# Optimization experiments

Measured on AMD Instinct MI355X. Metric: run time of the kernel, lower is better.

## Reference

```python
import jax, jax.numpy as jnp
import numpy as np

N_NODES = 50000
N_EDGES = 800000
IN_CH = 128
HEADS = 4
HID = 32  # per-head dim; heads*hid = 128
N_GRAPHS = 128


def setup_inputs() -> dict:
    key = jax.random.key(0)
    ks = jax.random.split(key, 32)
    d = {}
    d["x"] = jax.random.normal(ks[0], (N_NODES, IN_CH), dtype=jnp.float32)
    d["edge_index"] = jax.random.randint(ks[1], (2, N_EDGES), 0, N_NODES, dtype=jnp.int64)
    d["batch"] = jnp.sort(jax.random.randint(ks[2], (N_NODES,), 0, N_GRAPHS, dtype=jnp.int64))
    HD = HEADS * HID
    names = [("wq1", (IN_CH, HD)), ("bq1", (HD,)), ("wk1", (IN_CH, HD)), ("bk1", (HD,)),
             ("wv1", (IN_CH, HD)), ("bv1", (HD,)), ("ws1", (IN_CH, HD)), ("bs1", (HD,)),
             ("wq2", (HD, HD)), ("bq2", (HD,)), ("wk2", (HD, HD)), ("bk2", (HD,)),
             ("wv2", (HD, HD)), ("bv2", (HD,)), ("ws2", (HD, HD)), ("bs2", (HD,)),
             ("wl", (HD, HD)), ("bl", (HD,)), ("wl2", (HD, 1)), ("bl2", (1,))]
    for i, (nm, shp) in enumerate(names):
        d[nm] = jax.random.normal(ks[3 + i], shp, dtype=jnp.float32) * 0.05
    return d


def _transformer_conv(x, src, dst, wq, bq, wk, bk, wv, bv, ws, bs):
    """PyG TransformerConv: multi-head dot-product attention over edges,
    softmax normalized per destination node, plus linear root/skip term."""
    N = x.shape[0]
    q = (x @ wq + bq).reshape(N, HEADS, HID)
    k = (x @ wk + bk).reshape(N, HEADS, HID)
    v = (x @ wv + bv).reshape(N, HEADS, HID)
    # edge scores: [E, H]
    e = jnp.einsum('ehd,ehd->eh', q[dst], k[src]) * np.float32(1.0 / np.sqrt(HID))
    # segment softmax over incoming edges of each destination node
    m = jax.ops.segment_max(e, dst, num_segments=N)
    a = jnp.exp(e - m[dst])
    s = jax.ops.segment_sum(a, dst, num_segments=N)
    alpha = a / s[dst]  # [E, H]
    msg = alpha[:, :, None] * v[src]  # [E, H, D]
    out = jax.ops.segment_sum(msg, dst, num_segments=N).reshape(N, HEADS * HID)
    return out + x @ ws + bs  # root weight (skip) term


def reference(x, edge_index, batch,
              wq1, bq1, wk1, bk1, wv1, bv1, ws1, bs1,
              wq2, bq2, wk2, bk2, wv2, bv2, ws2, bs2,
              wl, bl, wl2, bl2):
    src, dst = edge_index[0], edge_index[1]
    h = _transformer_conv(x, src, dst, wq1, bq1, wk1, bk1, wv1, bv1, ws1, bs1)
    h = jax.nn.relu(h)
    h = _transformer_conv(h, src, dst, wq2, bq2, wk2, bk2, wv2, bv2, ws2, bs2)
    h = jax.nn.relu(h)
    h = h @ wl + bl
    h = h @ wl2 + bl2  # [N, 1]
    # global mean pool over graphs
    sums = jax.ops.segment_sum(h, batch, num_segments=N_GRAPHS)
    cnts = jax.ops.segment_sum(jnp.ones((h.shape[0], 1), h.dtype), batch, num_segments=N_GRAPHS)
    return sums / jnp.maximum(cnts, 1.0)
```

## Files before the change

kernel.cpp:

```cpp
#include <hip/hip_runtime.h>
#include <hip/hip_bf16.h>
#include <math.h>

#define NNODES 50000
#define NEDGES 800000
#define NGRAPHS 128
#define SCAN_B ((NNODES + 255) / 256)

typedef __attribute__((ext_vector_type(8))) short bf16x8;
typedef __attribute__((ext_vector_type(4))) float f32x4;

__device__ __forceinline__ unsigned short f2bf(float f) {
    unsigned int u = __float_as_uint(f);
    return (unsigned short)((u + 0x7FFFu + ((u >> 16) & 1u)) >> 16);
}
__device__ __forceinline__ unsigned pack2bf(float a, float b) {
    return (unsigned)f2bf(a) | ((unsigned)f2bf(b) << 16);
}
__device__ __forceinline__ float2 bf2f2(unsigned int u) {
    float2 f;
    f.x = __uint_as_float(u << 16);
    f.y = __uint_as_float(u & 0xFFFF0000u);
    return f;
}

__global__ void count_edges(const int* __restrict__ ei, int* __restrict__ cnt) {
    int e = blockIdx.x * 256 + threadIdx.x;
    if (e < NEDGES) atomicAdd(&cnt[ei[NEDGES + e]], 1);
}

__global__ __launch_bounds__(256)
void scan_pass1(const int* __restrict__ cnt, int* __restrict__ bsum) {
    const int t = threadIdx.x;
    const int i = blockIdx.x * 256 + t;
    int v = (i < NNODES) ? cnt[i] : 0;
#pragma unroll
    for (int off = 32; off > 0; off >>= 1) v += __shfl_xor(v, off, 64);
    __shared__ int ws[4];
    if ((t & 63) == 0) ws[t >> 6] = v;
    __syncthreads();
    if (t == 0) bsum[blockIdx.x] = ws[0] + ws[1] + ws[2] + ws[3];
}

__global__ __launch_bounds__(256)
void scan_pass2(const int* __restrict__ bsum, int* __restrict__ boff) {
    const int t = threadIdx.x;
    const int v = (t < SCAN_B) ? bsum[t] : 0;
    __shared__ int a[256];
    a[t] = v;
    __syncthreads();
    for (int off = 1; off < 256; off <<= 1) {
        const int u = (t >= off) ? a[t - off] : 0;
        __syncthreads();
        a[t] += u;
        __syncthreads();
    }
    if (t < SCAN_B) boff[t] = a[t] - v;
}

__global__ __launch_bounds__(256)
void scan_pass3(const int* __restrict__ cnt, const int* __restrict__ boff,
                int* __restrict__ rowptr, int* __restrict__ wpos) {
    const int t = threadIdx.x;
    const int i = blockIdx.x * 256 + t;
    const int v = (i < NNODES) ? cnt[i] : 0;
    __shared__ int a[256];
    a[t] = v;
    __syncthreads();
    for (int off = 1; off < 256; off <<= 1) {
        const int u = (t >= off) ? a[t - off] : 0;
        __syncthreads();
        a[t] += u;
        __syncthreads();
    }
    if (i < NNODES) {
        const int e = boff[blockIdx.x] + a[t] - v;
        rowptr[i] = e;
        wpos[i]   = e;
    }
    if (i == 0) rowptr[NNODES] = NEDGES;
}

__global__ void fill_csr(const int* __restrict__ ei, int* __restrict__ wpos,
                         int* __restrict__ colsrc) {
    int e = blockIdx.x * 256 + threadIdx.x;
    if (e < NEDGES) {
        int d = ei[NEDGES + e];
        int slot = atomicAdd(&wpos[d], 1);
        colsrc[slot] = ei[e];
    }
}

__global__ __launch_bounds__(256)
void prep_all(const float* __restrict__ wq1, const float* __restrict__ wk1,
              const float* __restrict__ wv1, const float* __restrict__ ws1,
              const float* __restrict__ wq2, const float* __restrict__ wk2,
              const float* __restrict__ wv2, const float* __restrict__ ws2,
              const float* __restrict__ wl, const float* __restrict__ bl,
              const float* __restrict__ wl2, const float* __restrict__ bl2,
              unsigned short* __restrict__ Wt, float* __restrict__ wf,
              float* __restrict__ bf) {
    const int b = blockIdx.x;
    if (b < 512) {
        const int layer = b >> 8;
        const int sel   = (b >> 6) & 3;
        const float* W = layer == 0
            ? (sel == 0 ? wq1 : sel == 1 ? wk1 : sel == 2 ? wv1 : ws1)
            : (sel == 0 ? wq2 : sel == 1 ? wk2 : sel == 2 ? wv2 : ws2);
        const int idx = (b & 63) * 256 + threadIdx.x;
        const int col = idx & 127;
        const int k   = idx >> 7;
        Wt[layer * 65536 + sel * 16384 + col * 128 + k] = f2bf(W[k * 128 + col]);
    } else {
        const int g = (b - 512) * 4 + (threadIdx.x >> 6);
        const int l = threadIdx.x & 63;
        if (g <= 128) {
            const float* row = (g < 128) ? &wl[g * 128] : bl;
            float s = row[l] * wl2[l] + row[64 + l] * wl2[64 + l];
#pragma unroll
            for (int off = 32; off > 0; off >>= 1) s += __shfl_xor(s, off, 64);
            if (l == 0) {
                if (g < 128) wf[g] = s;
                else         bf[0] = s + bl2[0];
            }
        }
    }
}

template <bool A_BF16>
__global__ __launch_bounds__(256, 3)
void gemm_qkvs(const void* __restrict__ Fv, const unsigned short* __restrict__ Wt,
               const float* __restrict__ bq, const float* __restrict__ bk,
               const float* __restrict__ bv, const float* __restrict__ bsk,
               unsigned short* __restrict__ Qb, unsigned short* __restrict__ Kb,
               unsigned short* __restrict__ Vb, unsigned short* __restrict__ Hb) {
    __shared__ __align__(16) unsigned short As[128][136];
    const int t    = threadIdx.x;
    const int m0   = blockIdx.x * 128;
    const int lane = t & 63;
    const int w    = t >> 6;
    const int l15  = lane & 15;
    const int lg   = lane >> 4;

    {
        const int row = t >> 1;
        const int kh  = (t & 1) * 64;
        const int gr  = min(m0 + row, NNODES - 1);
        if constexpr (A_BF16) {
            const unsigned short* src = &((const unsigned short*)Fv)[(size_t)gr * 128 + kh];
#pragma unroll
            for (int p = 0; p < 8; ++p)
                *(uint4*)&As[row][kh + p * 8] = *(const uint4*)&src[p * 8];
        } else {
            const float* src = &((const float*)Fv)[(size_t)gr * 128 + kh];
#pragma unroll
            for (int p = 0; p < 16; ++p) {
                const float4 v = *(const float4*)&src[p * 4];
                ushort4 u;
                u.x = f2bf(v.x); u.y = f2bf(v.y); u.z = f2bf(v.z); u.w = f2bf(v.w);
                *(ushort4*)&As[row][kh + p * 4] = u;
            }
        }
    }
    __syncthreads();

    for (int sl = 0; sl < 8; ++sl) {
        const int sel = sl >> 1;
        const int c0  = (sl & 1) * 64;
        const float* bias = sel == 0 ? bq : sel == 1 ? bk : sel == 2 ? bv : bsk;
        unsigned short* Ob = sel == 0 ? Qb : sel == 1 ? Kb : sel == 2 ? Vb : Hb;
        const unsigned short* Wsel = Wt + sel * 16384 + (size_t)c0 * 128;

        const float b0 = bias[c0 + l15];
        const float b1 = bias[c0 + 16 + l15];
        const float b2 = bias[c0 + 32 + l15];
        const float b3 = bias[c0 + 48 + l15];
        f32x4 a00 = {b0, b0, b0, b0}, a01 = {b1, b1, b1, b1},
              a02 = {b2, b2, b2, b2}, a03 = {b3, b3, b3, b3};
        f32x4 a10 = a00, a11 = a01, a12 = a02, a13 = a03;
#pragma unroll
        for (int ks = 0; ks < 4; ++ks) {
            const int kof = ks * 32 + lg * 8;
            const bf16x8 af0 = *(const bf16x8*)&As[w * 32 + l15][kof];
            const bf16x8 af1 = *(const bf16x8*)&As[w * 32 + 16 + l15][kof];
            const bf16x8 bf0 = *(const bf16x8*)&Wsel[(size_t)(l15) * 128 + kof];
            const bf16x8 bf1 = *(const bf16x8*)&Wsel[(size_t)(16 + l15) * 128 + kof];
            const bf16x8 bf2 = *(const bf16x8*)&Wsel[(size_t)(32 + l15) * 128 + kof];
            const bf16x8 bf3 = *(const bf16x8*)&Wsel[(size_t)(48 + l15) * 128 + kof];
            a00 = __builtin_amdgcn_mfma_f32_16x16x32_bf16(af0, bf0, a00, 0, 0, 0);
            a01 = __builtin_amdgcn_mfma_f32_16x16x32_bf16(af0, bf1, a01, 0, 0, 0);
            a02 = __builtin_amdgcn_mfma_f32_16x16x32_bf16(af0, bf2, a02, 0, 0, 0);
            a03 = __builtin_amdgcn_mfma_f32_16x16x32_bf16(af0, bf3, a03, 0, 0, 0);
            a10 = __builtin_amdgcn_mfma_f32_16x16x32_bf16(af1, bf0, a10, 0, 0, 0);
            a11 = __builtin_amdgcn_mfma_f32_16x16x32_bf16(af1, bf1, a11, 0, 0, 0);
            a12 = __builtin_amdgcn_mfma_f32_16x16x32_bf16(af1, bf2, a12, 0, 0, 0);
            a13 = __builtin_amdgcn_mfma_f32_16x16x32_bf16(af1, bf3, a13, 0, 0, 0);
        }

        const int r0 = m0 + w * 32 + lg * 4;
#define STB(ACC, RT, CT)                                                       \
        _Pragma("unroll")                                                      \
        for (int i = 0; i < 4; ++i) {                                          \
            const int gr = r0 + (RT) * 16 + i;                                 \
            if (gr < NNODES)                                                   \
                Ob[(size_t)gr * 128 + c0 + (CT) * 16 + l15] = f2bf(ACC[i]);    \
        }
        STB(a00, 0, 0) STB(a01, 0, 1) STB(a02, 0, 2) STB(a03, 0, 3)
        STB(a10, 1, 0) STB(a11, 1, 1) STB(a12, 1, 2) STB(a13, 1, 3)
#undef STB
    }
}

template <bool FUSE_HEAD>
__global__ __launch_bounds__(128)
void attn_agg(const unsigned short* __restrict__ Qb,
              const unsigned short* __restrict__ Kb,
              const unsigned short* __restrict__ Vb,
              unsigned short* __restrict__ Hb,
              const int* __restrict__ rowptr, const int* __restrict__ colsrc,
              const float* __restrict__ wf, float* __restrict__ r) {
    const int n = blockIdx.x * 2 + (threadIdx.x >> 6);
    const int l = threadIdx.x & 63;
    const int e = l >> 4;
    const int c = (l & 15) * 8;
    const uint4 qu = *(const uint4*)&Qb[(size_t)n * 128 + c];
    const float S = 0.17677669529663687f * 1.4426950408889634f;
    const float2 t01 = bf2f2(qu.x), t23 = bf2f2(qu.y);
    const float2 t45 = bf2f2(qu.z), t67 = bf2f2(qu.w);
    const float q0 = t01.x * S, q1 = t01.y * S, q2 = t23.x * S, q3 = t23.y * S;
    const float q4 = t45.x * S, q5 = t45.y * S, q6 = t67.x * S, q7 = t67.y * S;
    const int beg = rowptr[n], end = rowptr[n + 1];
    const int cnt = end - beg;

    float m = -INFINITY, s = 0.f;
    float a0 = 0.f, a1 = 0.f, a2 = 0.f, a3 = 0.f;
    float a4 = 0.f, a5 = 0.f, a6 = 0.f, a7 = 0.f;

    uint4 ku, vu;
    if (cnt > 0) {
        const int src = colsrc[min(beg + e, end - 1)];
        ku = *(const uint4*)&Kb[(size_t)src * 128 + c];
        vu = *(const uint4*)&Vb[(size_t)src * 128 + c];
    }
    for (int i = beg; i < end; i += 4) {
        const uint4 kc = ku, vc = vu;
        const bool valid = (i + e) < end;
        if (i + 4 < end) {
            const int srcN = colsrc[min(i + 4 + e, end - 1)];
            ku = *(const uint4*)&Kb[(size_t)srcN * 128 + c];
            vu = *(const uint4*)&Vb[(size_t)srcN * 128 + c];
        }
        const float2 k01 = bf2f2(kc.x), k23 = bf2f2(kc.y);
        const float2 k45 = bf2f2(kc.z), k67 = bf2f2(kc.w);
        float p = q0 * k01.x;
        p = fmaf(q1, k01.y, p); p = fmaf(q2, k23.x, p); p = fmaf(q3, k23.y, p);
        p = fmaf(q4, k45.x, p); p = fmaf(q5, k45.y, p); p = fmaf(q6, k67.x, p);
        p = fmaf(q7, k67.y, p);
        p += __shfl_xor(p, 2);
        p += __shfl_xor(p, 1);
        if (!valid) p = -INFINITY;
        if (!__all(p <= m + 8.f)) {
            float pm = fmaxf(p, __shfl_xor(p, 16));
            pm = fmaxf(pm, __shfl_xor(pm, 32));
            const float nm = fmaxf(m, pm);
            const float sc = exp2f(m - nm);
            s *= sc;
            a0 *= sc; a1 *= sc; a2 *= sc; a3 *= sc;
            a4 *= sc; a5 *= sc; a6 *= sc; a7 *= sc;
            m = nm;
        }
        const float w = exp2f(p - m);
        s += w;
        const float2 v01 = bf2f2(vc.x), v23 = bf2f2(vc.y);
        const float2 v45 = bf2f2(vc.z), v67 = bf2f2(vc.w);
        a0 = fmaf(w, v01.x, a0); a1 = fmaf(w, v01.y, a1);
        a2 = fmaf(w, v23.x, a2); a3 = fmaf(w, v23.y, a3);
        a4 = fmaf(w, v45.x, a4); a5 = fmaf(w, v45.y, a5);
        a6 = fmaf(w, v67.x, a6); a7 = fmaf(w, v67.y, a7);
    }
    s  += __shfl_xor(s, 16);  s  += __shfl_xor(s, 32);
    a0 += __shfl_xor(a0, 16); a0 += __shfl_xor(a0, 32);
    a1 += __shfl_xor(a1, 16); a1 += __shfl_xor(a1, 32);
    a2 += __shfl_xor(a2, 16); a2 += __shfl_xor(a2, 32);
    a3 += __shfl_xor(a3, 16); a3 += __shfl_xor(a3, 32);
    a4 += __shfl_xor(a4, 16); a4 += __shfl_xor(a4, 32);
    a5 += __shfl_xor(a5, 16); a5 += __shfl_xor(a5, 32);
    a6 += __shfl_xor(a6, 16); a6 += __shfl_xor(a6, 32);
    a7 += __shfl_xor(a7, 16); a7 += __shfl_xor(a7, 32);

    const uint4 hu = *(const uint4*)&Hb[(size_t)n * 128 + c];
    const float2 h01 = bf2f2(hu.x), h23 = bf2f2(hu.y);
    const float2 h45 = bf2f2(hu.z), h67 = bf2f2(hu.w);
    float o0 = h01.x, o1 = h01.y, o2 = h23.x, o3 = h23.y;
    float o4 = h45.x, o5 = h45.y, o6 = h67.x, o7 = h67.y;
    if (cnt > 0) {
        const float inv = 1.f / s;
        o0 = fmaf(a0, inv, o0); o1 = fmaf(a1, inv, o1);
        o2 = fmaf(a2, inv, o2); o3 = fmaf(a3, inv, o3);
        o4 = fmaf(a4, inv, o4); o5 = fmaf(a5, inv, o5);
        o6 = fmaf(a6, inv, o6); o7 = fmaf(a7, inv, o7);
    }
    o0 = fmaxf(o0, 0.f); o1 = fmaxf(o1, 0.f); o2 = fmaxf(o2, 0.f);
    o3 = fmaxf(o3, 0.f); o4 = fmaxf(o4, 0.f); o5 = fmaxf(o5, 0.f);
    o6 = fmaxf(o6, 0.f); o7 = fmaxf(o7, 0.f);
    if (!FUSE_HEAD) {
        if (e == 0) {
            uint4 o;
            o.x = pack2bf(o0, o1); o.y = pack2bf(o2, o3);
            o.z = pack2bf(o4, o5); o.w = pack2bf(o6, o7);
            *(uint4*)&Hb[(size_t)n * 128 + c] = o;
        }
    } else {
        const float4 wA = *(const float4*)&wf[c];
        const float4 wB = *(const float4*)&wf[c + 4];
        float val = fmaf(o0, wA.x, fmaf(o1, wA.y, fmaf(o2, wA.z, o3 * wA.w)));
        val = fmaf(o4, wB.x, fmaf(o5, wB.y, fmaf(o6, wB.z, fmaf(o7, wB.w, val))));
        val += __shfl_xor(val, 8);
        val += __shfl_xor(val, 4);
        val += __shfl_xor(val, 2);
        val += __shfl_xor(val, 1);
        if (l == 0) r[n] = val;
    }
}

__global__ __launch_bounds__(256)
void graph_pool(const float* __restrict__ r, const int* __restrict__ batch,
                const float* __restrict__ bf, float* __restrict__ out) {
    const int g = blockIdx.x;
    const int t = threadIdx.x;
    int lo = 0, hi = NNODES;
    while (lo < hi) { int mid = (lo + hi) >> 1; if (batch[mid] < g) lo = mid + 1; else hi = mid; }
    const int beg = lo;
    lo = beg; hi = NNODES;
    while (lo < hi) { int mid = (lo + hi) >> 1; if (batch[mid] < g + 1) lo = mid + 1; else hi = mid; }
    const int end = lo;

    float s = 0.f;
    for (int i = beg + t; i < end; i += 256) s += r[i];
#pragma unroll
    for (int off = 32; off > 0; off >>= 1) s += __shfl_xor(s, off, 64);
    __shared__ float pw[4];
    if ((t & 63) == 0) pw[t >> 6] = s;
    __syncthreads();
    if (t == 0) {
        const float cnt = (float)(end - beg);
        const float tot = pw[0] + pw[1] + pw[2] + pw[3] + cnt * bf[0];
        out[g] = tot / fmaxf(cnt, 1.f);
    }
}

extern "C" void kernel_launch(void* const* d_in, const int* in_sizes, int n_in,
                              void* d_out, int out_size, void* d_ws, size_t ws_size,
                              hipStream_t stream) {
    const float* x     = (const float*)d_in[0];
    const int*   ei    = (const int*)d_in[1];
    const int*   batch = (const int*)d_in[2];
    const float* wq1 = (const float*)d_in[3];  const float* bq1 = (const float*)d_in[4];
    const float* wk1 = (const float*)d_in[5];  const float* bk1 = (const float*)d_in[6];
    const float* wv1 = (const float*)d_in[7];  const float* bv1 = (const float*)d_in[8];
    const float* ws1 = (const float*)d_in[9];  const float* bs1 = (const float*)d_in[10];
    const float* wq2 = (const float*)d_in[11]; const float* bq2 = (const float*)d_in[12];
    const float* wk2 = (const float*)d_in[13]; const float* bk2 = (const float*)d_in[14];
    const float* wv2 = (const float*)d_in[15]; const float* bv2 = (const float*)d_in[16];
    const float* ws2 = (const float*)d_in[17]; const float* bs2 = (const float*)d_in[18];
    const float* wl  = (const float*)d_in[19]; const float* bl  = (const float*)d_in[20];
    const float* wl2 = (const float*)d_in[21]; const float* bl2 = (const float*)d_in[22];

    char* wsb = (char*)d_ws;
    size_t off = 0;
    auto carve = [&](size_t bytes) -> void* {
        void* p = wsb + off;
        off = (off + bytes + 255) & ~(size_t)255;
        return p;
    };
    const size_t NB = (size_t)NNODES * 128 * 2;
    unsigned short* Qb = (unsigned short*)carve(NB);
    unsigned short* Kb = (unsigned short*)carve(NB);
    unsigned short* Vb = (unsigned short*)carve(NB);
    unsigned short* H1 = (unsigned short*)carve(NB);
    unsigned short* H2 = (unsigned short*)carve(NB);
    int*   rowptr = (int*)carve((NNODES + 1) * sizeof(int));
    int*   wpos   = (int*)carve(NNODES * sizeof(int));
    int*   cnt    = (int*)carve(NNODES * sizeof(int));
    int*   colsrc = (int*)carve(NEDGES * sizeof(int));
    int*   bsum   = (int*)carve(256 * sizeof(int));
    int*   boff   = (int*)carve(256 * sizeof(int));
    float* wf     = (float*)carve(129 * sizeof(float));
    float* bf     = wf + 128;
    float* nodeval = (float*)carve(NNODES * sizeof(float));
    unsigned short* Wt = (unsigned short*)carve(131072 * sizeof(unsigned short));

    hipMemsetAsync(cnt, 0, NNODES * sizeof(int), stream);

    count_edges<<<(NEDGES + 255) / 256, 256, 0, stream>>>(ei, cnt);
    scan_pass1<<<SCAN_B, 256, 0, stream>>>(cnt, bsum);
    scan_pass2<<<1, 256, 0, stream>>>(bsum, boff);
    scan_pass3<<<SCAN_B, 256, 0, stream>>>(cnt, boff, rowptr, wpos);
    fill_csr<<<(NEDGES + 255) / 256, 256, 0, stream>>>(ei, wpos, colsrc);
    prep_all<<<545, 256, 0, stream>>>(wq1, wk1, wv1, ws1, wq2, wk2, wv2, ws2,
                                      wl, bl, wl2, bl2, Wt, wf, bf);

    const int ggrid = (NNODES + 127) / 128;
    const int agrid = NNODES / 2;
    gemm_qkvs<false><<<ggrid, 256, 0, stream>>>(x, Wt, bq1, bk1, bv1, bs1,
                                                Qb, Kb, Vb, H1);
    attn_agg<false><<<agrid, 128, 0, stream>>>(Qb, Kb, Vb, H1, rowptr, colsrc,
                                               nullptr, nullptr);
    gemm_qkvs<true><<<ggrid, 256, 0, stream>>>(H1, Wt + 65536, bq2, bk2, bv2, bs2,
                                               Qb, Kb, Vb, H2);
    attn_agg<true><<<agrid, 128, 0, stream>>>(Qb, Kb, Vb, H2, rowptr, colsrc,
                                              wf, nodeval);
    graph_pool<<<NGRAPHS, 256, 0, stream>>>(nodeval, batch, bf, (float*)d_out);
}
```

Before: 397.9 us.

## Fuse CSR build into one cooperative kernel and stage GEMM weights in LDS

Replaces the memset plus five CSR-building launches (count, three-pass scan, fill) with a single cooperative kernel that uses grid-wide syncs between phases, cutting launch overhead and small-kernel gaps. Separately, the QKVS GEMM now double-buffers each 64-column weight slice into shared memory instead of reading B fragments directly from global memory, and drops the occupancy hint from launch bounds. The extra LDS (two 64x136 bf16 buffers) and a barrier per slice may lower occupancy. The cooperative grid of 196 blocks must be co-resident for the grid syncs to work.

```diff
diff --git a/kernel.cpp b/kernel.cpp
--- a/kernel.cpp
+++ b/kernel.cpp
@@ -1,6 +1,9 @@
 #include <hip/hip_runtime.h>
 #include <hip/hip_bf16.h>
+#include <hip/hip_cooperative_groups.h>
 #include <math.h>
+
+namespace cg = cooperative_groups;
 
 #define NNODES 50000
 #define NEDGES 800000
@@ -24,29 +27,24 @@
     return f;
 }
 
-__global__ void count_edges(const int* __restrict__ ei, int* __restrict__ cnt) {
-    int e = blockIdx.x * 256 + threadIdx.x;
-    if (e < NEDGES) atomicAdd(&cnt[ei[NEDGES + e]], 1);
-}
-
 __global__ __launch_bounds__(256)
-void scan_pass1(const int* __restrict__ cnt, int* __restrict__ bsum) {
+void build_csr(const int* __restrict__ ei, int* __restrict__ cnt,
+               int* __restrict__ bsum, int* __restrict__ rowptr,
+               int* __restrict__ wpos, int* __restrict__ colsrc) {
+    cg::grid_group grid = cg::this_grid();
     const int t = threadIdx.x;
-    const int i = blockIdx.x * 256 + t;
-    int v = (i < NNODES) ? cnt[i] : 0;
-#pragma unroll
-    for (int off = 32; off > 0; off >>= 1) v += __shfl_xor(v, off, 64);
-    __shared__ int ws[4];
-    if ((t & 63) == 0) ws[t >> 6] = v;
-    __syncthreads();
-    if (t == 0) bsum[blockIdx.x] = ws[0] + ws[1] + ws[2] + ws[3];
-}
-
-__global__ __launch_bounds__(256)
-void scan_pass2(const int* __restrict__ bsum, int* __restrict__ boff) {
-    const int t = threadIdx.x;
-    const int v = (t < SCAN_B) ? bsum[t] : 0;
+    const int gid = blockIdx.x * 256 + t;
+    const int gstride = gridDim.x * 256;
+
+    for (int i = gid; i < NNODES; i += gstride) cnt[i] = 0;
+    grid.sync();
+
+    for (int e = gid; e < NEDGES; e += gstride)
+        atomicAdd(&cnt[ei[NEDGES + e]], 1);
+    grid.sync();
+
     __shared__ int a[256];
+    const int v = (gid < NNODES) ? cnt[gid] : 0;
     a[t] = v;
     __syncthreads();
     for (int off = 1; off < 256; off <<= 1) {
@@ -55,38 +53,28 @@
         a[t] += u;
         __syncthreads();
     }
-    if (t < SCAN_B) boff[t] = a[t] - v;
-}
-
-__global__ __launch_bounds__(256)
-void scan_pass3(const int* __restrict__ cnt, const int* __restrict__ boff,
-                int* __restrict__ rowptr, int* __restrict__ wpos) {
-    const int t = threadIdx.x;
-    const int i = blockIdx.x * 256 + t;
-    const int v = (i < NNODES) ? cnt[i] : 0;
-    __shared__ int a[256];
-    a[t] = v;
+    if (t == 255) bsum[blockIdx.x] = a[255];
+    grid.sync();
+
+    int s = 0;
+    for (int j = t; j < blockIdx.x; j += 256) s += bsum[j];
+#pragma unroll
+    for (int off = 32; off > 0; off >>= 1) s += __shfl_xor(s, off, 64);
+    __shared__ int pw[4];
+    if ((t & 63) == 0) pw[t >> 6] = s;
     __syncthreads();
-    for (int off = 1; off < 256; off <<= 1) {
-        const int u = (t >= off) ? a[t - off] : 0;
-        __syncthreads();
-        a[t] += u;
-        __syncthreads();
-    }
-    if (i < NNODES) {
-        const int e = boff[blockIdx.x] + a[t] - v;
-        rowptr[i] = e;
-        wpos[i]   = e;
-    }
-    if (i == 0) rowptr[NNODES] = NEDGES;
-}
-
-__global__ void fill_csr(const int* __restrict__ ei, int* __restrict__ wpos,
-                         int* __restrict__ colsrc) {
-    int e = blockIdx.x * 256 + threadIdx.x;
-    if (e < NEDGES) {
-        int d = ei[NEDGES + e];
-        int slot = atomicAdd(&wpos[d], 1);
+    const int boff = pw[0] + pw[1] + pw[2] + pw[3];
+    if (gid < NNODES) {
+        const int e = boff + a[t] - v;
+        rowptr[gid] = e;
+        wpos[gid]   = e;
+    }
+    if (gid == 0) rowptr[NNODES] = NEDGES;
+    grid.sync();
+
+    for (int e = gid; e < NEDGES; e += gstride) {
+        const int d = ei[NEDGES + e];
+        const int slot = atomicAdd(&wpos[d], 1);
         colsrc[slot] = ei[e];
     }
 }
@@ -128,13 +116,14 @@
 }
 
 template <bool A_BF16>
-__global__ __launch_bounds__(256, 3)
+__global__ __launch_bounds__(256)
 void gemm_qkvs(const void* __restrict__ Fv, const unsigned short* __restrict__ Wt,
                const float* __restrict__ bq, const float* __restrict__ bk,
                const float* __restrict__ bv, const float* __restrict__ bsk,
                unsigned short* __restrict__ Qb, unsigned short* __restrict__ Kb,
                unsigned short* __restrict__ Vb, unsigned short* __restrict__ Hb) {
     __shared__ __align__(16) unsigned short As[128][136];
+    __shared__ __align__(16) unsigned short Bt[2][64][136];
     const int t    = threadIdx.x;
     const int m0   = blockIdx.x * 128;
     const int lane = t & 63;
@@ -162,14 +151,28 @@
             }
         }
     }
+
+#define STAGE_B(BUF, SL)                                                       \
+    {                                                                          \
+        const int sel_ = (SL) >> 1, c0_ = ((SL) & 1) * 64;                     \
+        const int col = t >> 2, kb = (t & 3) * 32;                             \
+        const unsigned short* src = &Wt[sel_ * 16384 + (c0_ + col) * 128 + kb];\
+        _Pragma("unroll")                                                      \
+        for (int p = 0; p < 4; ++p)                                            \
+            *(uint4*)&Bt[BUF][col][kb + p * 8] = *(const uint4*)&src[p * 8];   \
+    }
+
+    STAGE_B(0, 0)
     __syncthreads();
 
     for (int sl = 0; sl < 8; ++sl) {
+        const int cur = sl & 1;
+        if (sl < 7) STAGE_B(cur ^ 1, sl + 1)
+
         const int sel = sl >> 1;
         const int c0  = (sl & 1) * 64;
         const float* bias = sel == 0 ? bq : sel == 1 ? bk : sel == 2 ? bv : bsk;
         unsigned short* Ob = sel == 0 ? Qb : sel == 1 ? Kb : sel == 2 ? Vb : Hb;
-        const unsigned short* Wsel = Wt + sel * 16384 + (size_t)c0 * 128;
 
         const float b0 = bias[c0 + l15];
         const float b1 = bias[c0 + 16 + l15];
@@ -183,10 +186,10 @@
             const int kof = ks * 32 + lg * 8;
             const bf16x8 af0 = *(const bf16x8*)&As[w * 32 + l15][kof];
             const bf16x8 af1 = *(const bf16x8*)&As[w * 32 + 16 + l15][kof];
-            const bf16x8 bf0 = *(const bf16x8*)&Wsel[(size_t)(l15) * 128 + kof];
-            const bf16x8 bf1 = *(const bf16x8*)&Wsel[(size_t)(16 + l15) * 128 + kof];
-            const bf16x8 bf2 = *(const bf16x8*)&Wsel[(size_t)(32 + l15) * 128 + kof];
-            const bf16x8 bf3 = *(const bf16x8*)&Wsel[(size_t)(48 + l15) * 128 + kof];
+            const bf16x8 bf0 = *(const bf16x8*)&Bt[cur][l15][kof];
+            const bf16x8 bf1 = *(const bf16x8*)&Bt[cur][16 + l15][kof];
+            const bf16x8 bf2 = *(const bf16x8*)&Bt[cur][32 + l15][kof];
+            const bf16x8 bf3 = *(const bf16x8*)&Bt[cur][48 + l15][kof];
             a00 = __builtin_amdgcn_mfma_f32_16x16x32_bf16(af0, bf0, a00, 0, 0, 0);
             a01 = __builtin_amdgcn_mfma_f32_16x16x32_bf16(af0, bf1, a01, 0, 0, 0);
             a02 = __builtin_amdgcn_mfma_f32_16x16x32_bf16(af0, bf2, a02, 0, 0, 0);
@@ -208,7 +211,9 @@
         STB(a00, 0, 0) STB(a01, 0, 1) STB(a02, 0, 2) STB(a03, 0, 3)
         STB(a10, 1, 0) STB(a11, 1, 1) STB(a12, 1, 2) STB(a13, 1, 3)
 #undef STB
-    }
+        __syncthreads();
+    }
+#undef STAGE_B
 }
 
 template <bool FUSE_HEAD>
@@ -384,19 +389,17 @@
     int*   cnt    = (int*)carve(NNODES * sizeof(int));
     int*   colsrc = (int*)carve(NEDGES * sizeof(int));
     int*   bsum   = (int*)carve(256 * sizeof(int));
-    int*   boff   = (int*)carve(256 * sizeof(int));
     float* wf     = (float*)carve(129 * sizeof(float));
     float* bf     = wf + 128;
     float* nodeval = (float*)carve(NNODES * sizeof(float));
     unsigned short* Wt = (unsigned short*)carve(131072 * sizeof(unsigned short));
 
-    hipMemsetAsync(cnt, 0, NNODES * sizeof(int), stream);
-
-    count_edges<<<(NEDGES + 255) / 256, 256, 0, stream>>>(ei, cnt);
-    scan_pass1<<<SCAN_B, 256, 0, stream>>>(cnt, bsum);
-    scan_pass2<<<1, 256, 0, stream>>>(bsum, boff);
-    scan_pass3<<<SCAN_B, 256, 0, stream>>>(cnt, boff, rowptr, wpos);
-    fill_csr<<<(NEDGES + 255) / 256, 256, 0, stream>>>(ei, wpos, colsrc);
+    {
+        void* args[] = {(void*)&ei, (void*)&cnt, (void*)&bsum,
+                        (void*)&rowptr, (void*)&wpos, (void*)&colsrc};
+        hipLaunchCooperativeKernel((void*)build_csr, dim3(SCAN_B), dim3(256),
+                                   args, 0, stream);
+    }
     prep_all<<<545, 256, 0, stream>>>(wq1, wk1, wv1, ws1, wq2, wk2, wv2, ws2,
                                       wl, bl, wl2, bl2, Wt, wf, bf);
 
```

New measurement: 471.6 us. 18.5% more time.
